# Performance work log

Measured on AMD Instinct MI355X. Metric: run time of the kernel, lower is better.

## Reference

```python
import jax, jax.numpy as jnp
import numpy as np

N = 100_000      # nodes
E = 1_000_000    # edges
F_IN = 32        # num_features
F_OUT = 32       # out_channels
K = 3            # num_filters (diffusion steps)


def setup_inputs() -> dict:
    key = jax.random.key(0)
    ks = jax.random.split(key, 12)
    d_in = F_IN + F_OUT  # gates see concat([X, H])
    s = 1.0 / np.sqrt(d_in)
    inp = {
        "x": jax.random.normal(ks[0], (N, F_IN), jnp.float32),
        "edge_index": jax.random.randint(ks[1], (2, E), 0, N, dtype=jnp.int32),
        "edge_weight": jax.random.uniform(ks[2], (E,), jnp.float32, 0.01, 1.0),
        "h": jnp.zeros((N, F_OUT), jnp.float32),
        "c": jnp.zeros((N, F_OUT), jnp.float32),
        # DConv weights: [2 directions, K hops, d_in, F_OUT] per gate
        "Wz": s * jax.random.normal(ks[3], (2, K, d_in, F_OUT), jnp.float32),
        "bz": jnp.zeros((F_OUT,), jnp.float32),
        "Wr": s * jax.random.normal(ks[4], (2, K, d_in, F_OUT), jnp.float32),
        "br": jnp.zeros((F_OUT,), jnp.float32),
        "Wh": s * jax.random.normal(ks[5], (2, K, d_in, F_OUT), jnp.float32),
        "bh": jnp.zeros((F_OUT,), jnp.float32),
        "Wl": s * jax.random.normal(ks[6], (F_OUT, 1), jnp.float32),
        "bl": jnp.zeros((1,), jnp.float32),
    }
    return inp


def _dconv(X, src, dst, ew, W, b):
    """Bidirectional K-hop diffusion conv (DCRNN DConv). X: [N, d_in]."""
    n = X.shape[0]
    deg_out = jax.ops.segment_sum(ew, src, num_segments=n)  # weighted out-degree
    deg_in = jax.ops.segment_sum(ew, dst, num_segments=n)   # weighted in-degree
    norm_out = ew / deg_out[src]  # D_out^{-1} W random walk
    norm_in = ew / deg_in[dst]    # D_in^{-1} W^T random walk

    def prop_out(v):  # forward diffusion: aggregate at dst from src
        return jax.ops.segment_sum(norm_out[:, None] * v[src], dst, num_segments=n)

    def prop_in(v):   # reverse diffusion: aggregate at src from dst
        return jax.ops.segment_sum(norm_in[:, None] * v[dst], src, num_segments=n)

    H = X @ W[0, 0] + X @ W[1, 0]
    Kk = W.shape[1]
    if Kk > 1:
        T0o = T0i = X
        T1o, T1i = prop_out(X), prop_in(X)
        H = H + T1o @ W[0, 1] + T1i @ W[1, 1]
        for k in range(2, Kk):
            T2o = 2.0 * prop_out(T1o) - T0o
            T2i = 2.0 * prop_in(T1i) - T0i
            H = H + T2o @ W[0, k] + T2i @ W[1, k]
            T0o, T1o = T1o, T2o
            T0i, T1i = T1i, T2i
    return H + b


def reference(x, edge_index, edge_weight, h, c, Wz, bz, Wr, br, Wh, bh, Wl, bl):
    src, dst = edge_index[0], edge_index[1]
    # wrapper passes H=None (h_1 = None) -> hidden state initialized to zeros
    H0 = jnp.zeros((x.shape[0], F_OUT), x.dtype)
    XH = jnp.concatenate([x, H0], axis=1)
    Z = jax.nn.sigmoid(_dconv(XH, src, dst, edge_weight, Wz, bz))
    R = jax.nn.sigmoid(_dconv(XH, src, dst, edge_weight, Wr, br))
    XRH = jnp.concatenate([x, R * H0], axis=1)
    H_tilde = jnp.tanh(_dconv(XRH, src, dst, edge_weight, Wh, bh))
    H = Z * H0 + (1.0 - Z) * H_tilde  # GRU update
    y = jax.nn.relu(H) @ Wl + bl      # relu + linear head
    return y
```

## Files before the change

kernel.cpp:

```cpp
#include <hip/hip_runtime.h>
#include <math.h>

#define NN 100000
#define NE 1000000
#define F 32
#define NBKT 196
#define BKT2 (2 * NBKT)
#define CAPB 5888
#define EB 4096
#define NTILE 6250
#define CONVB 1563

typedef unsigned short ushortT;
typedef unsigned int uintT;
typedef __attribute__((ext_vector_type(8))) short short8;
typedef __attribute__((ext_vector_type(4))) float f32x4;

__device__ inline float bfhi(uintT u)  { return __int_as_float(u & 0xffff0000u); }
__device__ inline float bflo(uintT u)  { return __int_as_float(u << 16); }
__device__ inline uintT f2bf(float f) {
    uintT u = __float_as_uint(f);
    return (u + 0x7fffu + ((u >> 16) & 1u)) >> 16;
}
__device__ inline uintT pack15(float f) {
    uintT u = __float_as_uint(f);
    return ((u + 0x7fffu + ((u >> 16) & 1u)) >> 16) & 0x7fffu;
}
__device__ inline float unpack15(uintT v) { return __int_as_float((v & 0x7fffu) << 16); }

__launch_bounds__(256)
__global__ void k_bucket(const int* __restrict__ ei, const float* __restrict__ ew,
                         int* __restrict__ cursor, uint2* __restrict__ stg) {
    __shared__ int cntL[BKT2], baseL[BKT2], curL[BKT2];

    const int tid = threadIdx.x;
    const int e0  = blockIdx.x * EB;

    for (int b = tid; b < BKT2; b += 256) { cntL[b] = 0; curL[b] = 0; }
    __syncthreads();

    int   rs[EB / 256];
    int   rd[EB / 256];
    uintT rw[EB / 256];
#pragma unroll
    for (int k = 0; k < EB / 256; ++k) {
        int gid = e0 + tid + k * 256;
        int s = -1, d = -1; uintT w = 0;
        if (gid < NE) {
            s = ei[gid]; d = ei[NE + gid]; w = pack15(ew[gid]);
            atomicAdd(&cntL[d >> 9], 1);
            atomicAdd(&cntL[NBKT + (s >> 9)], 1);
        }
        rs[k] = s; rd[k] = d; rw[k] = w;
    }
    __syncthreads();

    for (int b = tid; b < BKT2; b += 256)
        if (cntL[b] > 0) baseL[b] = atomicAdd(&cursor[b], cntL[b]);
    __syncthreads();

#pragma unroll
    for (int k = 0; k < EB / 256; ++k) {
        int s = rs[k];
        if (s < 0) continue;
        int d = rd[k]; uintT w = rw[k];
        int b0 = d >> 9;
        int p0 = baseL[b0] + atomicAdd(&curL[b0], 1);
        if (p0 < CAPB) stg[(size_t)b0 * CAPB + p0] = make_uint2(((uintT)s << 15) | w, (uintT)(d & 511));
        int b1 = NBKT + (s >> 9);
        int p1 = baseL[b1] + atomicAdd(&curL[b1], 1);
        if (p1 < CAPB) stg[(size_t)b1 * CAPB + p1] = make_uint2(((uintT)d << 15) | w, (uintT)(s & 511));
    }
}

__launch_bounds__(256)
__global__ void k_csr(const int* __restrict__ cursor, const uint2* __restrict__ stg,
                      uintT* __restrict__ entF, int2* __restrict__ meta,
                      float* __restrict__ rdeg) {
    __shared__ int   ncnt[512];
    __shared__ int   nbase[512];
    __shared__ int   ncur[512];
    __shared__ float wsum[512];
    __shared__ int   wavesum[4];

    const int b   = blockIdx.x;
    const int tid = threadIdx.x;
    const int dir = (b >= NBKT) ? 1 : 0;
    const int n0  = (dir ? (b - NBKT) : b) << 9;
    const int c   = min(cursor[b], CAPB);
    const uint2* S = stg + (size_t)b * CAPB;

    for (int l = tid; l < 512; l += 256) { ncnt[l] = 0; ncur[l] = 0; wsum[l] = 0.f; }
    __syncthreads();

    for (int i = tid; i < c; i += 256) {
        uint2 it = S[i];
        atomicAdd(&ncnt[it.y], 1);
        atomicAdd(&wsum[it.y], unpack15(it.x));
    }
    __syncthreads();

    int v0 = ncnt[2 * tid], v1 = ncnt[2 * tid + 1];
    int sp = v0 + v1;
    int lane = tid & 63, wid = tid >> 6;
    int incl = sp;
#pragma unroll
    for (int o = 1; o < 64; o <<= 1) {
        int t = __shfl_up(incl, o, 64);
        if (lane >= o) incl += t;
    }
    if (lane == 63) wavesum[wid] = incl;
    __syncthreads();
    int woff = 0;
    for (int wq = 0; wq < wid; ++wq) woff += wavesum[wq];
    int ex = incl - sp + woff;
    nbase[2 * tid] = ex;
    nbase[2 * tid + 1] = ex + v0;
    __syncthreads();

    const int rb = b * CAPB;
    for (int l = tid; l < 512; l += 256) {
        int node = n0 + l;
        if (node < NN) {
            int seg = dir * NN + node;
            meta[seg] = make_int2(rb + nbase[l], ncnt[l]);
            float s = wsum[l];
            rdeg[seg] = 1.0f / ((s > 0.f) ? s : 1.0f);
        }
    }
    __syncthreads();

    for (int i = tid; i < c; i += 256) {
        uint2 it = S[i];
        int r = atomicAdd(&ncur[it.y], 1);
        entF[rb + nbase[it.y] + r] = it.x;
    }
}

__launch_bounds__(256)
__global__ void k_prep(const float* __restrict__ x, ushortT* __restrict__ xbr,
                       const float* __restrict__ Wz, const float* __restrict__ Wh,
                       ushortT* __restrict__ wfrag) {
    if (blockIdx.x < CONVB) {
        int i = blockIdx.x * 256 + threadIdx.x;
        if (i >= NN * F / 8) return;
        const float4* p = (const float4*)x + (long)i * 2;
        float4 a = p[0], b = p[1];
        uint4 o;
        o.x = f2bf(a.x) | (f2bf(a.y) << 16);
        o.y = f2bf(a.z) | (f2bf(a.w) << 16);
        o.z = f2bf(b.x) | (f2bf(b.y) << 16);
        o.w = f2bf(b.z) | (f2bf(b.w) << 16);
        ((uint4*)xbr)[i] = o;
        return;
    }
    int gid = (blockIdx.x - CONVB) * 256 + threadIdx.x;
    if (gid >= 20 * 512) return;
    int f = gid >> 9, rem = gid & 511;
    int l = rem >> 3, r = rem & 7;
    int kc = f >> 2, nt = f & 3;
    int n = nt * 16 + (l & 15);
    int fi = (l >> 4) * 8 + r;
    int jc = n & 31;
    const float* W = (n >= 32) ? Wh : Wz;
#define WDK(d, k) W[((((d) * 3 + (k)) * 64) + fi) * 32 + jc]
    float v;
    if      (kc == 0) v = WDK(0,0) + WDK(1,0) - WDK(0,2) - WDK(1,2);
    else if (kc == 1) v = WDK(0,1);
    else if (kc == 2) v = WDK(1,1);
    else if (kc == 3) v = 2.0f * WDK(0,2);
    else              v = 2.0f * WDK(1,2);
#undef WDK
    wfrag[gid] = (ushortT)f2bf(v);
}

__launch_bounds__(256)
__global__ void k_hop(const int2* __restrict__ meta, const uintT* __restrict__ entF,
                      const float* __restrict__ rdeg,
                      const ushortT* __restrict__ fo, const ushortT* __restrict__ fi,
                      ushortT* __restrict__ oo, ushortT* __restrict__ oi) {
    const int dir = blockIdx.x & 1;
    const int n   = (blockIdx.x >> 1) * 32 + (threadIdx.x >> 3);
    if (n >= NN) return;
    const int q   = threadIdx.x & 7;
    const int2 m  = meta[dir * NN + n];
    const int opp = dir ? 0 : NN;
    const ushortT* __restrict__ feat = dir ? fi : fo;

    float ax = 0.f, ay = 0.f, az = 0.f, aw = 0.f;
    const int end = m.x + m.y, last = end - 1;
    for (int p = m.x; p < end; p += 8) {
        float nms[8]; uint2 vs[8];
#pragma unroll
        for (int k = 0; k < 8; ++k) {
            int i  = p + k;
            int ic = min(i, last);
            uintT en = entF[ic];
            int idx = (int)(en >> 15);
            float nm = unpack15(en) * rdeg[opp + idx];
            vs[k]  = *(const uint2*)(feat + (long)idx * F + q * 4);
            nms[k] = (i < end) ? nm : 0.f;
        }
#pragma unroll
        for (int k = 0; k < 8; ++k) {
            ax += nms[k] * bflo(vs[k].x);
            ay += nms[k] * bfhi(vs[k].x);
            az += nms[k] * bflo(vs[k].y);
            aw += nms[k] * bfhi(vs[k].y);
        }
    }
    uint2 o = make_uint2(f2bf(ax) | (f2bf(ay) << 16), f2bf(az) | (f2bf(aw) << 16));
    *(uint2*)((dir ? oi : oo) + (long)n * F + q * 4) = o;
}

__launch_bounds__(256)
__global__ void k_final(const ushortT* __restrict__ xb,
                        const ushortT* __restrict__ t1o, const ushortT* __restrict__ t1i,
                        const ushortT* __restrict__ p2o, const ushortT* __restrict__ p2i,
                        const ushortT* __restrict__ wfrag,
                        const float* __restrict__ bz, const float* __restrict__ bh,
                        const float* __restrict__ Wl, const float* __restrict__ bl,
                        float* __restrict__ y, int nwaves) {
    const int lane = threadIdx.x & 63;
    const int wgid = blockIdx.x * 4 + (threadIdx.x >> 6);
    const int quad = lane >> 4;
    const int c0   = lane & 15;

    union U8 { uint4 u; short8 s; };

    short8 bfr[20];
#pragma unroll
    for (int f = 0; f < 20; ++f) {
        U8 t; t.u = *(const uint4*)(wfrag + f * 512 + lane * 8);
        bfr[f] = t.s;
    }

    const float bz0 = bz[c0], bz1 = bz[c0 + 16];
    const float bh0 = bh[c0], bh1 = bh[c0 + 16];
    const float wl0 = Wl[c0], wl1 = Wl[c0 + 16];
    const float blv = bl[0];

    const ushortT* srcs[5] = {xb, t1o, t1i, p2o, p2i};

    for (int t = wgid; t < NTILE; t += nwaves) {
        const long off = (long)t * 16 * F + (long)c0 * F + quad * 8;
        f32x4 a0 = {0.f, 0.f, 0.f, 0.f}, a1 = a0, a2 = a0, a3 = a0;
#pragma unroll
        for (int kc = 0; kc < 5; ++kc) {
            U8 av; av.u = *(const uint4*)(srcs[kc] + off);
            a0 = __builtin_amdgcn_mfma_f32_16x16x32_bf16(av.s, bfr[kc * 4 + 0], a0, 0, 0, 0);
            a1 = __builtin_amdgcn_mfma_f32_16x16x32_bf16(av.s, bfr[kc * 4 + 1], a1, 0, 0, 0);
            a2 = __builtin_amdgcn_mfma_f32_16x16x32_bf16(av.s, bfr[kc * 4 + 2], a2, 0, 0, 0);
            a3 = __builtin_amdgcn_mfma_f32_16x16x32_bf16(av.s, bfr[kc * 4 + 3], a3, 0, 0, 0);
        }
        float res[4];
#pragma unroll
        for (int r = 0; r < 4; ++r) {
            float gz = a0[r] + bz0, gh = a2[r] + bh0;
            float z  = 1.0f / (1.0f + __expf(-gz));
            float e2 = __expf(2.0f * gh);
            float ht = 1.0f - 2.0f / (e2 + 1.0f);
            float v  = fmaxf((1.0f - z) * ht, 0.0f) * wl0;
            gz = a1[r] + bz1; gh = a3[r] + bh1;
            z  = 1.0f / (1.0f + __expf(-gz));
            e2 = __expf(2.0f * gh);
            ht = 1.0f - 2.0f / (e2 + 1.0f);
            v += fmaxf((1.0f - z) * ht, 0.0f) * wl1;
            res[r] = v;
        }
#pragma unroll
        for (int o = 1; o < 16; o <<= 1) {
            res[0] += __shfl_xor(res[0], o, 64);
            res[1] += __shfl_xor(res[1], o, 64);
            res[2] += __shfl_xor(res[2], o, 64);
            res[3] += __shfl_xor(res[3], o, 64);
        }
        if (c0 == 0) {
            f32x4 out = {res[0] + blv, res[1] + blv, res[2] + blv, res[3] + blv};
            *(f32x4*)(y + t * 16 + quad * 4) = out;
        }
    }
}

extern "C" void kernel_launch(void* const* d_in, const int* in_sizes, int n_in,
                              void* d_out, int out_size, void* d_ws, size_t ws_size,
                              hipStream_t stream) {
    const float* x  = (const float*)d_in[0];
    const int*   ei = (const int*)  d_in[1];
    const float* ew = (const float*)d_in[2];
    const float* Wz = (const float*)d_in[5];
    const float* bz = (const float*)d_in[6];
    const float* Wh = (const float*)d_in[9];
    const float* bh = (const float*)d_in[10];
    const float* Wl = (const float*)d_in[11];
    const float* bl = (const float*)d_in[12];
    float* y = (float*)d_out;

    const size_t segs = 2 * NN;
    const long   NFW  = (long)NN * F;
    int*     cursor = (int*)d_ws;
    int2*    meta   = (int2*)(cursor + 400);
    float*   rdeg   = (float*)(meta + segs);
    uintT*   entF   = (uintT*)(rdeg + segs);
    ushortT* wfrag  = (ushortT*)(entF + (size_t)BKT2 * CAPB);
    ushortT* xbr    = wfrag + 10240;
    ushortT* t1o    = xbr + NFW;
    ushortT* t1i    = t1o + NFW;
    ushortT* p2o    = t1i + NFW;
    ushortT* p2i    = p2o + NFW;
    uint2*   stg    = (uint2*)t1o;

    hipMemsetAsync(cursor, 0, BKT2 * sizeof(int), stream);

    const int B = 256;
    k_prep<<<CONVB + 40, B, 0, stream>>>(x, xbr, Wz, Wh, wfrag);
    k_bucket<<<(NE + EB - 1) / EB, B, 0, stream>>>(ei, ew, cursor, stg);
    k_csr<<<BKT2, B, 0, stream>>>(cursor, stg, entF, meta, rdeg);
    k_hop<<<2 * ((NN + 31) / 32), B, 0, stream>>>(meta, entF, rdeg, xbr, xbr, t1o, t1i);
    k_hop<<<2 * ((NN + 31) / 32), B, 0, stream>>>(meta, entF, rdeg, t1o, t1i, p2o, p2i);
    const int fblocks = 512;
    k_final<<<fblocks, B, 0, stream>>>(xbr, t1o, t1i, p2o, p2i, wfrag,
                                       bz, bh, Wl, bl, y, fblocks * 4);
}
```

Before: 224.4 us.

## Compute weighted degrees with global atomics in bucketing, widen CSR blocks

Weighted in- and out-degree sums move out of k_csr's shared-memory float atomics and into k_bucket, which now issues global float atomicAdds per edge into a zeroed deg array. k_csr then only inverts the degrees in place and runs 512 threads (one per local node), which simplifies its prefix scan. EB drops from 4096 to 1024 so k_bucket launches more blocks. The staging buffer moves to its own region after p2i instead of aliasing t1o. The cost is two million scattered global float atomics and a larger memset, and float atomic order makes the degree sums nondeterministic.

```diff
diff --git a/kernel.cpp b/kernel.cpp
--- a/kernel.cpp
+++ b/kernel.cpp
@@ -7,7 +7,7 @@
 #define NBKT 196
 #define BKT2 (2 * NBKT)
 #define CAPB 5888
-#define EB 4096
+#define EB 1024
 #define NTILE 6250
 #define CONVB 1563
 
@@ -30,7 +30,8 @@
 
 __launch_bounds__(256)
 __global__ void k_bucket(const int* __restrict__ ei, const float* __restrict__ ew,
-                         int* __restrict__ cursor, uint2* __restrict__ stg) {
+                         int* __restrict__ cursor, uint2* __restrict__ stg,
+                         float* __restrict__ deg) {
     __shared__ int cntL[BKT2], baseL[BKT2], curL[BKT2];
 
     const int tid = threadIdx.x;
@@ -50,6 +51,9 @@
             s = ei[gid]; d = ei[NE + gid]; w = pack15(ew[gid]);
             atomicAdd(&cntL[d >> 9], 1);
             atomicAdd(&cntL[NBKT + (s >> 9)], 1);
+            float wf = unpack15(w);
+            atomicAdd(&deg[d], wf);
+            atomicAdd(&deg[NN + s], wf);
         }
         rs[k] = s; rd[k] = d; rw[k] = w;
     }
@@ -73,15 +77,14 @@
     }
 }
 
-__launch_bounds__(256)
+__launch_bounds__(512)
 __global__ void k_csr(const int* __restrict__ cursor, const uint2* __restrict__ stg,
                       uintT* __restrict__ entF, int2* __restrict__ meta,
                       float* __restrict__ rdeg) {
-    __shared__ int   ncnt[512];
-    __shared__ int   nbase[512];
-    __shared__ int   ncur[512];
-    __shared__ float wsum[512];
-    __shared__ int   wavesum[4];
+    __shared__ int ncnt[512];
+    __shared__ int nbase[512];
+    __shared__ int ncur[512];
+    __shared__ int wavesum[8];
 
     const int b   = blockIdx.x;
     const int tid = threadIdx.x;
@@ -90,18 +93,22 @@
     const int c   = min(cursor[b], CAPB);
     const uint2* S = stg + (size_t)b * CAPB;
 
-    for (int l = tid; l < 512; l += 256) { ncnt[l] = 0; ncur[l] = 0; wsum[l] = 0.f; }
-    __syncthreads();
-
-    for (int i = tid; i < c; i += 256) {
-        uint2 it = S[i];
-        atomicAdd(&ncnt[it.y], 1);
-        atomicAdd(&wsum[it.y], unpack15(it.x));
-    }
-    __syncthreads();
-
-    int v0 = ncnt[2 * tid], v1 = ncnt[2 * tid + 1];
-    int sp = v0 + v1;
+    {
+        int g = b * 512 + tid;
+        if (g < 2 * NN) {
+            float s = rdeg[g];
+            rdeg[g] = (s > 0.f) ? 1.0f / s : 1.0f;
+        }
+    }
+
+    ncnt[tid] = 0; ncur[tid] = 0;
+    __syncthreads();
+
+    for (int i = tid; i < c; i += 512)
+        atomicAdd(&ncnt[S[i].y], 1);
+    __syncthreads();
+
+    int sp   = ncnt[tid];
     int lane = tid & 63, wid = tid >> 6;
     int incl = sp;
 #pragma unroll
@@ -113,24 +120,17 @@
     __syncthreads();
     int woff = 0;
     for (int wq = 0; wq < wid; ++wq) woff += wavesum[wq];
-    int ex = incl - sp + woff;
-    nbase[2 * tid] = ex;
-    nbase[2 * tid + 1] = ex + v0;
+    nbase[tid] = incl - sp + woff;
     __syncthreads();
 
     const int rb = b * CAPB;
-    for (int l = tid; l < 512; l += 256) {
-        int node = n0 + l;
-        if (node < NN) {
-            int seg = dir * NN + node;
-            meta[seg] = make_int2(rb + nbase[l], ncnt[l]);
-            float s = wsum[l];
-            rdeg[seg] = 1.0f / ((s > 0.f) ? s : 1.0f);
-        }
-    }
-    __syncthreads();
-
-    for (int i = tid; i < c; i += 256) {
+    {
+        int node = n0 + tid;
+        if (node < NN)
+            meta[dir * NN + node] = make_int2(rb + nbase[tid], ncnt[tid]);
+    }
+
+    for (int i = tid; i < c; i += 512) {
         uint2 it = S[i];
         int r = atomicAdd(&ncur[it.y], 1);
         entF[rb + nbase[it.y] + r] = it.x;
@@ -296,28 +296,27 @@
     const float* bl = (const float*)d_in[12];
     float* y = (float*)d_out;
 
-    const size_t segs = 2 * NN;
-    const long   NFW  = (long)NN * F;
+    const long NFW = (long)NN * F;
     int*     cursor = (int*)d_ws;
-    int2*    meta   = (int2*)(cursor + 400);
-    float*   rdeg   = (float*)(meta + segs);
-    uintT*   entF   = (uintT*)(rdeg + segs);
+    float*   deg    = (float*)(cursor + 512);
+    int2*    meta   = (int2*)(deg + 2 * NN);
+    uintT*   entF   = (uintT*)(meta + 2 * NN);
     ushortT* wfrag  = (ushortT*)(entF + (size_t)BKT2 * CAPB);
     ushortT* xbr    = wfrag + 10240;
     ushortT* t1o    = xbr + NFW;
     ushortT* t1i    = t1o + NFW;
     ushortT* p2o    = t1i + NFW;
     ushortT* p2i    = p2o + NFW;
-    uint2*   stg    = (uint2*)t1o;
-
-    hipMemsetAsync(cursor, 0, BKT2 * sizeof(int), stream);
+    uint2*   stg    = (uint2*)(p2i + NFW);
+
+    hipMemsetAsync(d_ws, 0, (512 + 2 * NN) * sizeof(int), stream);
 
     const int B = 256;
     k_prep<<<CONVB + 40, B, 0, stream>>>(x, xbr, Wz, Wh, wfrag);
-    k_bucket<<<(NE + EB - 1) / EB, B, 0, stream>>>(ei, ew, cursor, stg);
-    k_csr<<<BKT2, B, 0, stream>>>(cursor, stg, entF, meta, rdeg);
-    k_hop<<<2 * ((NN + 31) / 32), B, 0, stream>>>(meta, entF, rdeg, xbr, xbr, t1o, t1i);
-    k_hop<<<2 * ((NN + 31) / 32), B, 0, stream>>>(meta, entF, rdeg, t1o, t1i, p2o, p2i);
+    k_bucket<<<(NE + EB - 1) / EB, B, 0, stream>>>(ei, ew, cursor, stg, deg);
+    k_csr<<<BKT2, 512, 0, stream>>>(cursor, stg, entF, meta, deg);
+    k_hop<<<2 * ((NN + 31) / 32), B, 0, stream>>>(meta, entF, deg, xbr, xbr, t1o, t1i);
+    k_hop<<<2 * ((NN + 31) / 32), B, 0, stream>>>(meta, entF, deg, t1o, t1i, p2o, p2i);
     const int fblocks = 512;
     k_final<<<fblocks, B, 0, stream>>>(xbr, t1o, t1i, p2o, p2i, wfrag,
                                        bz, bh, Wl, bl, y, fblocks * 4);
```

Measured after the change: 310.2 us. 38.3% more time.
